# Performance work log

Hardware: AMD Instinct MI355X
Metric: run time of the kernel (lower is better)

## Reference

```python
import jax, jax.numpy as jnp
import numpy as np

K = 16  # kNN neighbors


def _knn(xb, k):
    # xb: [N, H] -> [N, k] nearest-neighbor indices (self excluded)
    sq = jnp.sum(xb * xb, axis=-1)
    d = sq[:, None] + sq[None, :] - 2.0 * (xb @ xb.T)  # squared distances [N, N]
    n = xb.shape[0]
    big = jnp.asarray(1e30, d.dtype)
    d = d + jnp.eye(n, dtype=d.dtype) * big  # mask self-loops
    _, idx = jax.lax.top_k(-d, k)
    return idx


def _edgeconv(h, W0, b0, W1, b1, k):
    # Dynamic kNN graph on current features + EdgeConv with 2-layer MLP, aggr='add'
    idx = jax.vmap(lambda xb: _knn(xb, k))(h)                 # [B, N, k]
    xj = jax.vmap(lambda xb, ib: xb[ib])(h, idx)              # [B, N, k, H] gather neighbors
    xi = jnp.broadcast_to(h[:, :, None, :], xj.shape)         # [B, N, k, H]
    m = jnp.concatenate([xi, xj - xi], axis=-1)               # [B, N, k, 2H]
    e = jax.nn.elu(m @ W0 + b0)
    e = jax.nn.elu(e @ W1 + b1)
    return jnp.sum(e, axis=2)                                 # 'add' aggregation over neighbors


def _forward(x, W_in0, b_in0, W_in1, b_in1, W_in2, b_in2,
             W_e0, b_e0, W_e1, b_e1,
             W_o0, b_o0, W_o1, b_o1, W_o2, b_o2):
    # input network (in_layers=3)
    h = jax.nn.elu(x @ W_in0 + b_in0)
    h = jax.nn.elu(h @ W_in1 + b_in1)
    h = jax.nn.elu(h @ W_in2 + b_in2)
    # agg_layers=2 blocks of dynamic-kNN EdgeConv
    for l in range(W_e0.shape[0]):
        h = _edgeconv(h, W_e0[l], b_e0[l], W_e1[l], b_e1[l], K)
    # global max pool over nodes of each graph (pool='max')
    g = jnp.max(h, axis=1)                                    # [B, H]
    # output network (out_layers=3)
    g = jax.nn.elu(g @ W_o0 + b_o0)
    g = jax.nn.elu(g @ W_o1 + b_o1)
    logits = g @ W_o2 + b_o2
    return jax.nn.log_softmax(logits, axis=1)


def setup_inputs() -> dict:
    key = jax.random.key(0)
    ks = jax.random.split(key, 8)
    B, N, F, H, C, A = 128, 512, 5, 64, 10, 2
    s = jnp.float32(0.1)

    def w(k, shape):
        return jax.random.normal(k, shape, jnp.float32) * s

    return {
        'x': jax.random.normal(ks[0], (B, N, F), jnp.float32),
        'W_in0': w(ks[1], (F, H)), 'b_in0': jnp.zeros((H,), jnp.float32),
        'W_in1': w(ks[2], (H, H)), 'b_in1': jnp.zeros((H,), jnp.float32),
        'W_in2': w(ks[3], (H, H)), 'b_in2': jnp.zeros((H,), jnp.float32),
        'W_e0': w(ks[4], (A, 2 * H, H)), 'b_e0': jnp.zeros((A, H), jnp.float32),
        'W_e1': w(ks[5], (A, H, H)), 'b_e1': jnp.zeros((A, H), jnp.float32),
        'W_o0': w(ks[6], (H, H)), 'b_o0': jnp.zeros((H,), jnp.float32),
        'W_o1': w(ks[7], (H, H)), 'b_o1': jnp.zeros((H,), jnp.float32),
        'W_o2': w(jax.random.fold_in(key, 99), (H, C)), 'b_o2': jnp.zeros((C,), jnp.float32),
    }


def reference(x, W_in0, b_in0, W_in1, b_in1, W_in2, b_in2,
              W_e0, b_e0, W_e1, b_e1,
              W_o0, b_o0, W_o1, b_o1, W_o2, b_o2):
    return _forward(x, W_in0, b_in0, W_in1, b_in1, W_in2, b_in2,
                    W_e0, b_e0, W_e1, b_e1,
                    W_o0, b_o0, W_o1, b_o1, W_o2, b_o2)
```

## Files before the change

kernel.cpp:

```cpp
#include <hip/hip_runtime.h>
#include <hip/hip_fp16.h>
#include <cmath>

typedef _Float16 f16;
typedef _Float16 f16x8 __attribute__((ext_vector_type(8)));
typedef float f32x4 __attribute__((ext_vector_type(4)));

#define B_ 128
#define N_ 512
#define H_ 64
#define K_ 16

__device__ __forceinline__ float elu_(float x) { return x > 0.f ? x : (__expf(x) - 1.f); }
__device__ __forceinline__ unsigned umin_(unsigned a, unsigned b) { return a < b ? a : b; }
__device__ __forceinline__ unsigned umax_(unsigned a, unsigned b) { return a > b ? a : b; }
__device__ __forceinline__ f32x4 mfma16(f16x8 a, f16x8 b, f32x4 c) {
    return __builtin_amdgcn_mfma_f32_16x16x32_f16(a, b, c, 0, 0, 0);
}
__device__ __forceinline__ f32x4 splat4(float v) { f32x4 r; r[0]=v; r[1]=v; r[2]=v; r[3]=v; return r; }
__device__ __forceinline__ unsigned mbcnt_(unsigned long long mask) {
    return __builtin_amdgcn_mbcnt_hi((unsigned)(mask >> 32),
           __builtin_amdgcn_mbcnt_lo((unsigned)mask, 0u));
}
__device__ __forceinline__ f16 hexp_(f16 x) {
    __half h = *(__half*)&x; h = hexp(h); return *(f16*)&h;
}
__device__ __forceinline__ f16x8 elu8h_(f16x8 x) {
    f16x8 z; f16x8 one;
    #pragma unroll
    for (int i = 0; i < 8; ++i) { z[i] = (f16)0.f; one[i] = (f16)1.f; }
    f16x8 mx = __builtin_elementwise_max(x, z);
    f16x8 mn = __builtin_elementwise_min(x, z);
    f16x8 e;
    #pragma unroll
    for (int i = 0; i < 8; ++i) e[i] = hexp_(mn[i]);
    return mx + e - one;
}
__device__ __forceinline__ unsigned wmax64_(unsigned v) {
    v = umax_(v, (unsigned)__builtin_amdgcn_update_dpp(0, (int)v, 0x111, 0xf, 0xf, true));
    v = umax_(v, (unsigned)__builtin_amdgcn_update_dpp(0, (int)v, 0x112, 0xf, 0xf, true));
    v = umax_(v, (unsigned)__builtin_amdgcn_update_dpp(0, (int)v, 0x114, 0xf, 0xf, true));
    v = umax_(v, (unsigned)__builtin_amdgcn_update_dpp(0, (int)v, 0x118, 0xf, 0xf, true));
    v = umax_(v, (unsigned)__builtin_amdgcn_update_dpp(0, (int)v, 0x142, 0xa, 0xf, true));
    v = umax_(v, (unsigned)__builtin_amdgcn_update_dpp(0, (int)v, 0x143, 0xc, 0xf, true));
    return (unsigned)__builtin_amdgcn_readlane((int)v, 63);
}
__device__ __forceinline__ float rsum16lo_(float x) {
    x += __int_as_float(__builtin_amdgcn_update_dpp(0, __float_as_int(x), 0x101, 0xf, 0xf, true));
    x += __int_as_float(__builtin_amdgcn_update_dpp(0, __float_as_int(x), 0x102, 0xf, 0xf, true));
    x += __int_as_float(__builtin_amdgcn_update_dpp(0, __float_as_int(x), 0x104, 0xf, 0xf, true));
    x += __int_as_float(__builtin_amdgcn_update_dpp(0, __float_as_int(x), 0x108, 0xf, 0xf, true));
    return x;
}

__global__ __launch_bounds__(256) void mlp_kernel(const float* __restrict__ x,
        const float* __restrict__ W0, const float* __restrict__ b0,
        const float* __restrict__ W1, const float* __restrict__ b1,
        const float* __restrict__ W2, const float* __restrict__ b2,
        f16* __restrict__ hout, float* __restrict__ sqout)
{
    __shared__ f16 tile[4][16*72];
    __shared__ f16 w1t[64*80];
    __shared__ f16 w2t[64*80];
    const int tid = threadIdx.x;
    const int lane = tid & 63, wid = tid >> 6;
    const int m = lane & 15, q = lane >> 4;
    const int rowbase = blockIdx.x*64 + wid*16;
    f16* tw = tile[wid];

    {
        const int k  = tid >> 2;
        const int n0 = (tid & 3) << 4;
        #pragma unroll
        for (int jj = 0; jj < 4; ++jj) {
            const float4 v1 = *(const float4*)(W1 + k*64 + n0 + jj*4);
            const float4 v2 = *(const float4*)(W2 + k*64 + n0 + jj*4);
            const int nb = n0 + jj*4;
            w1t[(nb+0)*80 + k] = (f16)v1.x; w1t[(nb+1)*80 + k] = (f16)v1.y;
            w1t[(nb+2)*80 + k] = (f16)v1.z; w1t[(nb+3)*80 + k] = (f16)v1.w;
            w2t[(nb+0)*80 + k] = (f16)v2.x; w2t[(nb+1)*80 + k] = (f16)v2.y;
            w2t[(nb+2)*80 + k] = (f16)v2.z; w2t[(nb+3)*80 + k] = (f16)v2.w;
        }
    }

    f16x8 af0, af1;
    {
        const float* xp = x + (size_t)(rowbase + m)*5;
        #pragma unroll
        for (int jj = 0; jj < 8; ++jj) { int k = q*8+jj; af0[jj] = (k < 5) ? (f16)xp[k] : (f16)0.f; }
    }
    f32x4 acc[4];
    #pragma unroll
    for (int t = 0; t < 4; ++t) {
        f16x8 bf;
        #pragma unroll
        for (int jj = 0; jj < 8; ++jj) { int k = q*8+jj; bf[jj] = (k < 5) ? (f16)W0[k*64 + t*16+m] : (f16)0.f; }
        acc[t] = splat4(b0[t*16+m]);
        acc[t] = mfma16(af0, bf, acc[t]);
    }
    #pragma unroll
    for (int t = 0; t < 4; ++t)
        #pragma unroll
        for (int r = 0; r < 4; ++r)
            tw[(q*4+r)*72 + t*16+m] = (f16)elu_(acc[t][r]);
    af0 = *(const f16x8*)(tw + m*72 + q*8);
    af1 = *(const f16x8*)(tw + m*72 + q*8 + 32);
    __syncthreads();

    #pragma unroll
    for (int t = 0; t < 4; ++t) {
        f16x8 bfa = *(const f16x8*)(w1t + (t*16+m)*80 + q*8);
        f16x8 bfb = *(const f16x8*)(w1t + (t*16+m)*80 + q*8 + 32);
        acc[t] = splat4(b1[t*16+m]);
        acc[t] = mfma16(af0, bfa, acc[t]);
        acc[t] = mfma16(af1, bfb, acc[t]);
    }
    #pragma unroll
    for (int t = 0; t < 4; ++t)
        #pragma unroll
        for (int r = 0; r < 4; ++r)
            tw[(q*4+r)*72 + t*16+m] = (f16)elu_(acc[t][r]);
    af0 = *(const f16x8*)(tw + m*72 + q*8);
    af1 = *(const f16x8*)(tw + m*72 + q*8 + 32);

    #pragma unroll
    for (int t = 0; t < 4; ++t) {
        f16x8 bfa = *(const f16x8*)(w2t + (t*16+m)*80 + q*8);
        f16x8 bfb = *(const f16x8*)(w2t + (t*16+m)*80 + q*8 + 32);
        acc[t] = splat4(b2[t*16+m]);
        acc[t] = mfma16(af0, bfa, acc[t]);
        acc[t] = mfma16(af1, bfb, acc[t]);
    }
    float s[4] = {0.f,0.f,0.f,0.f};
    #pragma unroll
    for (int t = 0; t < 4; ++t)
        #pragma unroll
        for (int r = 0; r < 4; ++r) {
            float v = elu_(acc[t][r]);
            hout[(size_t)(rowbase + q*4 + r)*64 + t*16 + m] = (f16)v;
            s[r] += v*v;
        }
    #pragma unroll
    for (int r = 0; r < 4; ++r) s[r] = rsum16lo_(s[r]);
    if (m == 0) {
        #pragma unroll
        for (int r = 0; r < 4; ++r) sqout[rowbase + q*4 + r] = s[r];
    }
}

__global__ __launch_bounds__(512, 8) void knn_kernel(const f16* __restrict__ hin,
        const float* __restrict__ sq, int* __restrict__ idxout,
        const float* __restrict__ We, const float* __restrict__ be,
        f16* __restrict__ Pout, f16* __restrict__ Qout)
{
    __shared__ unsigned keys[16*512];
    const int lane = threadIdx.x & 63;
    const int wid  = threadIdx.x >> 6;
    const int m = lane & 15, q = lane >> 4;
    const int b  = blockIdx.x >> 5;
    const int rt = blockIdx.x & 31;
    const int rowbase = rt*16;
    const f16* hb = hin + (size_t)b*N_*H_;
    const float* sqb = sq + b*N_;

    f16x8 af0, af1;
    {
        const f16* Ap = hb + (size_t)(rowbase + m)*64 + q*8;
        af0 = *(const f16x8*)Ap;
        af1 = *(const f16x8*)(Ap + 32);
    }
    const int colb0 = wid*16;
    f16x8 bf0[4], bf1[4];
    float sc[4];
    #pragma unroll
    for (int cti = 0; cti < 4; ++cti) {
        const f16* Bp = hb + (size_t)(colb0 + cti*128 + m)*64 + q*8;
        bf0[cti] = *(const f16x8*)Bp;
        bf1[cti] = *(const f16x8*)(Bp + 32);
        sc[cti] = sqb[colb0 + cti*128 + m];
    }
    int base_r[4];
    #pragma unroll
    for (int r = 0; r < 4; ++r) {
        const int row = q*4 + r;
        base_r[r] = row*512 + ((colb0 + m) ^ (row << 1));
    }
    #pragma unroll
    for (int cti = 0; cti < 4; ++cti) {
        f32x4 acc = splat4(0.f);
        acc = mfma16(af0, bf0[cti], acc);
        acc = mfma16(af1, bf1[cti], acc);
        #pragma unroll
        for (int r = 0; r < 4; ++r) {
            float d = fmaf(-2.f, acc[r], sc[cti]);
            unsigned u = __float_as_uint(d);
            u ^= (0x80000000u | (unsigned)((int)u >> 31));
            unsigned key = (u & 0xFFFFFE00u) | (unsigned)(colb0 + cti*128 + m);
            keys[base_r[r] + cti*128] = key;
        }
    }
    __syncthreads();

    unsigned kk[2][8];
    #pragma unroll
    for (int rr = 0; rr < 2; ++rr) {
        const int ri = wid*2 + rr;
        *(uint4*)&kk[rr][0] = *(const uint4*)(keys + ri*512 + lane*4);
        *(uint4*)&kk[rr][4] = *(const uint4*)(keys + ri*512 + 256 + lane*4);
    }
    unsigned* scr = keys + wid*2*512;

    unsigned v[2];
    #pragma unroll
    for (int rr = 0; rr < 2; ++rr) {
        unsigned mn = kk[rr][0];
        #pragma unroll
        for (int s2 = 1; s2 < 8; ++s2) mn = umin_(mn, kk[rr][s2]);
        v[rr] = mn;
    }
    unsigned T[2] = {0u,0u};
    #pragma unroll
    for (int bit = 31; bit >= 9; --bit) {
        #pragma unroll
        for (int rr = 0; rr < 2; ++rr) {
            unsigned cand = T[rr] | (1u << bit);
            int c = __popcll(__ballot(v[rr] < cand));
            T[rr] = (c < 17) ? cand : T[rr];
        }
    }
    T[0] |= 511u; T[1] |= 511u;

    unsigned cnt[2];
    #pragma unroll
    for (int rr = 0; rr < 2; ++rr) {
        unsigned long long bal[8];
        #pragma unroll
        for (int s2 = 0; s2 < 8; ++s2) bal[s2] = __ballot(kk[rr][s2] <= T[rr]);
        unsigned base = 0;
        #pragma unroll
        for (int s2 = 0; s2 < 8; ++s2) {
            if (kk[rr][s2] <= T[rr]) {
                unsigned pos = base + mbcnt_(bal[s2]);
                if (pos < 64u) scr[rr*64 + pos] = kk[rr][s2];
            }
            base += (unsigned)__popcll(bal[s2]);
        }
        cnt[rr] = base;
    }

    #pragma unroll
    for (int rr = 0; rr < 2; ++rr) {
        const unsigned cc_ = umin_(cnt[rr], 64u);
        const int ri = wid*2 + rr;
        const unsigned rowglob = (unsigned)(rowbase + ri);
        bool act = lane < (int)cc_;
        unsigned mv = act ? scr[rr*64 + lane] : 0u;
        if (act && (mv & 511u) == rowglob) { act = false; mv = 0u; }
        int e = __popcll(__ballot(act)) - 16;
        while (e > 0) {
            unsigned mx = wmax64_(mv);
            if (mv == mx) { act = false; mv = 0u; }
            --e;
        }
        int* outp = idxout + ((size_t)b*N_ + rowglob)*K_;
        unsigned long long bal = __ballot(act);
        unsigned rank = mbcnt_(bal);
        if (act) outp[rank] = (int)(mv & 511u);
    }

    {
        const int t = wid & 3;
        f32x4 acc = (wid < 4) ? splat4(be[t*16+m]) : splat4(0.f);
        #pragma unroll
        for (int cc = 0; cc < 2; ++cc) {
            const f16x8 afc = cc ? af1 : af0;
            f16x8 bb;
            if (wid < 4) {
                #pragma unroll
                for (int jj = 0; jj < 8; ++jj) {
                    float wa = We[(q*8+jj+32*cc)*64 + t*16+m];
                    float wb = We[(q*8+jj+32*cc+64)*64 + t*16+m];
                    bb[jj] = (f16)(wa - wb);
                }
            } else {
                #pragma unroll
                for (int jj = 0; jj < 8; ++jj)
                    bb[jj] = (f16)We[(q*8+jj+32*cc+64)*64 + t*16+m];
            }
            acc = mfma16(afc, bb, acc);
        }
        f16* outp = (wid < 4) ? Pout : Qout;
        #pragma unroll
        for (int r = 0; r < 4; ++r)
            outp[((size_t)b*N_ + rowbase + q*4 + r)*64 + t*16 + m] = (f16)acc[r];
    }
}

__device__ __forceinline__ void edge_node_(size_t r0, f16x8 pa, f16x8 pb,
        f16x8 qa, f16x8 qb, const f16x8 (&bf)[2][4], const float (&bcol)[4],
        f16* __restrict__ out, float* __restrict__ sqout, int lane)
{
    f16x8 af0 = elu8h_(pa + qa);
    f16x8 af1 = elu8h_(pb + qb);
    f32x4 acc[4];
    #pragma unroll
    for (int t = 0; t < 4; ++t) acc[t] = splat4(bcol[t]);
    #pragma unroll
    for (int t = 0; t < 4; ++t) acc[t] = mfma16(af0, bf[0][t], acc[t]);
    #pragma unroll
    for (int t = 0; t < 4; ++t) acc[t] = mfma16(af1, bf[1][t], acc[t]);
    float ssum = 0.f;
    #pragma unroll
    for (int t = 0; t < 4; ++t) {
        float s = elu_(acc[t][0]) + elu_(acc[t][1]) + elu_(acc[t][2]) + elu_(acc[t][3]);
        s += __shfl_xor(s, 16);
        s += __shfl_xor(s, 32);
        if (lane < 16) out[r0*64 + t*16 + lane] = (f16)s;
        ssum += s*s;
    }
    ssum = rsum16lo_(ssum);
    if (lane == 0) sqout[r0] = ssum;
}

__global__ __launch_bounds__(256, 4) void edge_kernel(const f16* __restrict__ P,
        const f16* __restrict__ Q, const int* __restrict__ idx,
        const float* __restrict__ W1, const float* __restrict__ b1,
        f16* __restrict__ out, float* __restrict__ sqout)
{
    const int lane = threadIdx.x & 63;
    const int wid  = threadIdx.x >> 6;
    const int m = lane & 15, q = lane >> 4;

    f16x8 bf[2][4];
    #pragma unroll
    for (int cc = 0; cc < 2; ++cc)
        #pragma unroll
        for (int t = 0; t < 4; ++t)
            #pragma unroll
            for (int jj = 0; jj < 8; ++jj)
                bf[cc][t][jj] = (f16)W1[(q*8 + jj + 32*cc)*64 + t*16 + m];
    float bcol[4];
    #pragma unroll
    for (int t = 0; t < 4; ++t) bcol[t] = b1[t*16 + m];

    const int node0 = blockIdx.x*16 + wid*4;
    const int gbase = node0 & ~(N_-1);
    const int c0a = q*8, c0b = q*8 + 32;
    int jv[4];
    #pragma unroll
    for (int i = 0; i < 4; ++i) jv[i] = idx[(size_t)(node0 + i)*K_ + m];

    f16x8 pA[4], pB[4], qA[4], qB[4];
    #pragma unroll
    for (int k2 = 0; k2 < 4; ++k2) {
        const size_t r0 = (size_t)(node0 + k2);
        const size_t g0 = (size_t)(gbase + jv[k2]);
        pA[k2] = *(const f16x8*)(P + r0*64 + c0a);
        pB[k2] = *(const f16x8*)(P + r0*64 + c0b);
        qA[k2] = *(const f16x8*)(Q + g0*64 + c0a);
        qB[k2] = *(const f16x8*)(Q + g0*64 + c0b);
    }
    #pragma unroll
    for (int k2 = 0; k2 < 4; ++k2)
        edge_node_((size_t)(node0 + k2), pA[k2], pB[k2], qA[k2], qB[k2],
                   bf, bcol, out, sqout, lane);
}

__global__ __launch_bounds__(512) void final_kernel(const f16* __restrict__ hin,
        const float* __restrict__ Wo0, const float* __restrict__ bo0,
        const float* __restrict__ Wo1, const float* __restrict__ bo1,
        const float* __restrict__ Wo2, const float* __restrict__ bo2,
        float* __restrict__ out)
{
    __shared__ float smax[64][64];
    __shared__ float g0[64], g1[64], g2[64], part[8][64], lg[10];
    const int t = threadIdx.x;
    const int b = blockIdx.x;
    const int cg = t & 7, rg = t >> 3;

    float mx[8];
    #pragma unroll
    for (int e = 0; e < 8; ++e) mx[e] = -3.0e38f;
    #pragma unroll
    for (int i = 0; i < 8; ++i) {
        const int row = rg + i*64;
        f16x8 vv = *(const f16x8*)(hin + ((size_t)b*N_ + row)*64 + cg*8);
        #pragma unroll
        for (int e = 0; e < 8; ++e) mx[e] = fmaxf(mx[e], (float)vv[e]);
    }
    #pragma unroll
    for (int e = 0; e < 8; ++e) smax[rg][cg*8 + e] = mx[e];
    __syncthreads();
    for (int s = 32; s >= 1; s >>= 1) {
        if (rg < s) {
            #pragma unroll
            for (int e = 0; e < 8; ++e)
                smax[rg][cg*8+e] = fmaxf(smax[rg][cg*8+e], smax[rg+s][cg*8+e]);
        }
        __syncthreads();
    }
    if (t < 64) g0[t] = smax[0][t];
    __syncthreads();

    const int j = t & 63, p = t >> 6;
    {
        float a = 0.f;
        #pragma unroll
        for (int c = 0; c < 8; ++c) a += g0[p*8 + c]*Wo0[(p*8 + c)*64 + j];
        part[p][j] = a;
    }
    __syncthreads();
    if (t < 64) {
        float a = bo0[t];
        #pragma unroll
        for (int p2 = 0; p2 < 8; ++p2) a += part[p2][t];
        g1[t] = elu_(a);
    }
    __syncthreads();
    {
        float a = 0.f;
        #pragma unroll
        for (int c = 0; c < 8; ++c) a += g1[p*8 + c]*Wo1[(p*8 + c)*64 + j];
        part[p][j] = a;
    }
    __syncthreads();
    if (t < 64) {
        float a = bo1[t];
        #pragma unroll
        for (int p2 = 0; p2 < 8; ++p2) a += part[p2][t];
        g2[t] = elu_(a);
    }
    __syncthreads();
    if (t < 10) { float a = bo2[t]; for (int c = 0; c < 64; ++c) a += g2[c]*Wo2[c*10 + t]; lg[t] = a; }
    __syncthreads();
    if (t == 0) {
        float mxl = lg[0];
        for (int i = 1; i < 10; ++i) mxl = fmaxf(mxl, lg[i]);
        float s = 0.f;
        for (int i = 0; i < 10; ++i) s += expf(lg[i] - mxl);
        const float lse = mxl + logf(s);
        for (int i = 0; i < 10; ++i) out[b*10 + i] = lg[i] - lse;
    }
}

extern "C" void kernel_launch(void* const* d_in, const int* in_sizes, int n_in,
                              void* d_out, int out_size, void* d_ws, size_t ws_size,
                              hipStream_t stream) {
    const float* x     = (const float*)d_in[0];
    const float* W_in0 = (const float*)d_in[1];
    const float* b_in0 = (const float*)d_in[2];
    const float* W_in1 = (const float*)d_in[3];
    const float* b_in1 = (const float*)d_in[4];
    const float* W_in2 = (const float*)d_in[5];
    const float* b_in2 = (const float*)d_in[6];
    const float* W_e0  = (const float*)d_in[7];
    const float* b_e0  = (const float*)d_in[8];
    const float* W_e1  = (const float*)d_in[9];
    const float* b_e1  = (const float*)d_in[10];
    const float* Wo0   = (const float*)d_in[11];
    const float* bo0   = (const float*)d_in[12];
    const float* Wo1   = (const float*)d_in[13];
    const float* bo1   = (const float*)d_in[14];
    const float* Wo2   = (const float*)d_in[15];
    const float* bo2   = (const float*)d_in[16];

    char* ws = (char*)d_ws;
    f16*    hA   = (f16*)(ws);
    f16*    hB   = (f16*)(ws + 8388608);
    f16*    Pb   = (f16*)(ws + 16777216);
    f16*    Qb   = (f16*)(ws + 25165824);
    int*    idxb = (int*)(ws + 33554432);
    float*  sqb  = (float*)(ws + 37748736);

    mlp_kernel<<<1024, 256, 0, stream>>>(x, W_in0, b_in0, W_in1, b_in1, W_in2, b_in2,
                                         hA, sqb);
    knn_kernel<<<4096, 512, 0, stream>>>(hA, sqb, idxb, W_e0, b_e0, Pb, Qb);
    edge_kernel<<<4096, 256, 0, stream>>>(Pb, Qb, idxb, W_e1, b_e1, hB, sqb);
    knn_kernel<<<4096, 512, 0, stream>>>(hB, sqb, idxb, W_e0 + 8192, b_e0 + 64, Pb, Qb);
    edge_kernel<<<4096, 256, 0, stream>>>(Pb, Qb, idxb, W_e1 + 4096, b_e1 + 64, hA, sqb);

    final_kernel<<<128, 512, 0, stream>>>(hA, Wo0, bo0, Wo1, bo1, Wo2, bo2, (float*)d_out);
}
```

Baseline: 279.6 us.

## Pretranspose edge weights to fp16 and swizzle block order across XCDs

A new single-block prep kernel converts the EdgeConv weights to fp16 once per call, precomputing Wa-Wb and transposing them. The knn and edge kernels then load each weight fragment as one 16-byte vector instead of doing eight strided fp32 loads per fragment. Block indices in both kernels are also remapped so consecutive blocks of the same graph land on the same XCD, which should improve L2 locality for that graph's features. The cost is one extra serial launch that runs on a single block.

New measurement: 303.2 us. +8.4%, slower.

```diff
diff --git a/kernel.cpp b/kernel.cpp
--- a/kernel.cpp
+++ b/kernel.cpp
@@ -53,6 +53,26 @@
     return x;
 }
 
+__global__ __launch_bounds__(256) void prep_kernel(const float* __restrict__ We0,
+        const float* __restrict__ We1,
+        f16* __restrict__ PW, f16* __restrict__ QW, f16* __restrict__ W1T)
+{
+    const int t = threadIdx.x;
+    #pragma unroll
+    for (int l = 0; l < 2; ++l) {
+        const float* A  = We0 + l*8192;
+        const float* B1 = We1 + l*4096;
+        for (int i = t; i < 4096; i += 256) {
+            const int n = i >> 6, k = i & 63;
+            const float wa = A[k*64 + n];
+            const float wb = A[(k+64)*64 + n];
+            PW [l*4096 + n*64 + k] = (f16)(wa - wb);
+            QW [l*4096 + n*64 + k] = (f16)wb;
+            W1T[l*4096 + n*64 + k] = (f16)B1[k*64 + n];
+        }
+    }
+}
+
 __global__ __launch_bounds__(256) void mlp_kernel(const float* __restrict__ x,
         const float* __restrict__ W0, const float* __restrict__ b0,
         const float* __restrict__ W1, const float* __restrict__ b1,
@@ -150,15 +170,17 @@
 
 __global__ __launch_bounds__(512, 8) void knn_kernel(const f16* __restrict__ hin,
         const float* __restrict__ sq, int* __restrict__ idxout,
-        const float* __restrict__ We, const float* __restrict__ be,
+        const f16* __restrict__ PWl, const float* __restrict__ be,
+        const f16* __restrict__ QWl,
         f16* __restrict__ Pout, f16* __restrict__ Qout)
 {
     __shared__ unsigned keys[16*512];
     const int lane = threadIdx.x & 63;
     const int wid  = threadIdx.x >> 6;
     const int m = lane & 15, q = lane >> 4;
-    const int b  = blockIdx.x >> 5;
-    const int rt = blockIdx.x & 31;
+    const int bid = ((blockIdx.x & 7) << 9) | (blockIdx.x >> 3);
+    const int b  = bid >> 5;
+    const int rt = bid & 31;
     const int rowbase = rt*16;
     const f16* hb = hin + (size_t)b*N_*H_;
     const float* sqb = sq + b*N_;
@@ -270,23 +292,13 @@
 
     {
         const int t = wid & 3;
-        f32x4 acc = (wid < 4) ? splat4(be[t*16+m]) : splat4(0.f);
+        const int n = t*16 + m;
+        f32x4 acc = (wid < 4) ? splat4(be[n]) : splat4(0.f);
+        const f16* Wp = (wid < 4) ? PWl : QWl;
         #pragma unroll
         for (int cc = 0; cc < 2; ++cc) {
             const f16x8 afc = cc ? af1 : af0;
-            f16x8 bb;
-            if (wid < 4) {
-                #pragma unroll
-                for (int jj = 0; jj < 8; ++jj) {
-                    float wa = We[(q*8+jj+32*cc)*64 + t*16+m];
-                    float wb = We[(q*8+jj+32*cc+64)*64 + t*16+m];
-                    bb[jj] = (f16)(wa - wb);
-                }
-            } else {
-                #pragma unroll
-                for (int jj = 0; jj < 8; ++jj)
-                    bb[jj] = (f16)We[(q*8+jj+32*cc+64)*64 + t*16+m];
-            }
+            const f16x8 bb = *(const f16x8*)(Wp + n*64 + cc*32 + q*8);
             acc = mfma16(afc, bb, acc);
         }
         f16* outp = (wid < 4) ? Pout : Qout;
@@ -324,7 +336,7 @@
 
 __global__ __launch_bounds__(256, 4) void edge_kernel(const f16* __restrict__ P,
         const f16* __restrict__ Q, const int* __restrict__ idx,
-        const float* __restrict__ W1, const float* __restrict__ b1,
+        const f16* __restrict__ W1T, const float* __restrict__ b1,
         f16* __restrict__ out, float* __restrict__ sqout)
 {
     const int lane = threadIdx.x & 63;
@@ -336,14 +348,13 @@
     for (int cc = 0; cc < 2; ++cc)
         #pragma unroll
         for (int t = 0; t < 4; ++t)
-            #pragma unroll
-            for (int jj = 0; jj < 8; ++jj)
-                bf[cc][t][jj] = (f16)W1[(q*8 + jj + 32*cc)*64 + t*16 + m];
+            bf[cc][t] = *(const f16x8*)(W1T + (t*16 + m)*64 + cc*32 + q*8);
     float bcol[4];
     #pragma unroll
     for (int t = 0; t < 4; ++t) bcol[t] = b1[t*16 + m];
 
-    const int node0 = blockIdx.x*16 + wid*4;
+    const int bid = ((blockIdx.x & 7) << 9) | (blockIdx.x >> 3);
+    const int node0 = bid*16 + wid*4;
     const int gbase = node0 & ~(N_-1);
     const int c0a = q*8, c0b = q*8 + 32;
     int jv[4];
@@ -471,13 +482,17 @@
     f16*    Qb   = (f16*)(ws + 25165824);
     int*    idxb = (int*)(ws + 33554432);
     float*  sqb  = (float*)(ws + 37748736);
-
+    f16*    PW   = (f16*)(ws + 38010880);
+    f16*    QW   = (f16*)(ws + 38027264);
+    f16*    W1T  = (f16*)(ws + 38043648);
+
+    prep_kernel<<<1, 256, 0, stream>>>(W_e0, W_e1, PW, QW, W1T);
     mlp_kernel<<<1024, 256, 0, stream>>>(x, W_in0, b_in0, W_in1, b_in1, W_in2, b_in2,
                                          hA, sqb);
-    knn_kernel<<<4096, 512, 0, stream>>>(hA, sqb, idxb, W_e0, b_e0, Pb, Qb);
-    edge_kernel<<<4096, 256, 0, stream>>>(Pb, Qb, idxb, W_e1, b_e1, hB, sqb);
-    knn_kernel<<<4096, 512, 0, stream>>>(hB, sqb, idxb, W_e0 + 8192, b_e0 + 64, Pb, Qb);
-    edge_kernel<<<4096, 256, 0, stream>>>(Pb, Qb, idxb, W_e1 + 4096, b_e1 + 64, hA, sqb);
+    knn_kernel<<<4096, 512, 0, stream>>>(hA, sqb, idxb, PW, b_e0, QW, Pb, Qb);
+    edge_kernel<<<4096, 256, 0, stream>>>(Pb, Qb, idxb, W1T, b_e1, hB, sqb);
+    knn_kernel<<<4096, 512, 0, stream>>>(hB, sqb, idxb, PW + 4096, b_e0 + 64, QW + 4096, Pb, Qb);
+    edge_kernel<<<4096, 256, 0, stream>>>(Pb, Qb, idxb, W1T + 4096, b_e1 + 64, hA, sqb);
 
     final_kernel<<<128, 512, 0, stream>>>(hA, Wo0, bo0, Wo1, bo1, Wo2, bo2, (float*)d_out);
 }
```
